# Performance work log

Measured on AMD Instinct MI355X. Metric: run time of the kernel, lower is better.

Reference implementation:

```python
import jax, jax.numpy as jnp
import numpy as np

B, T, C, NH = 4, 2048, 1024, 16
HS = C // NH  # 64


def setup_inputs() -> dict:
    key = jax.random.key(0)
    ks = jax.random.split(key, 3)
    x = jax.random.normal(ks[0], (B, T, C), dtype=jnp.float32)
    w_attn = jax.random.normal(ks[1], (C, 3 * C), dtype=jnp.float32) * (1.0 / np.sqrt(C))
    b_attn = jnp.zeros((3 * C,), dtype=jnp.float32)
    w_proj = jax.random.normal(ks[2], (C, C), dtype=jnp.float32) * (1.0 / np.sqrt(C))
    b_proj = jnp.zeros((C,), dtype=jnp.float32)
    return {"x": x, "w_attn": w_attn, "b_attn": b_attn, "w_proj": w_proj, "b_proj": b_proj}


def reference(x, w_attn, b_attn, w_proj, b_proj):
    Bx, Tx, Cx = x.shape
    qkv = x @ w_attn + b_attn                      # (B,T,3C)
    q, k, v = jnp.split(qkv, 3, axis=2)
    # faithful to torch: view(B,T,hs,nh).transpose(1,3) -> (B,nh,hs,T)
    def to_heads(t):
        return jnp.transpose(t.reshape(Bx, Tx, HS, NH), (0, 3, 2, 1))
    q, k, v = to_heads(q), to_heads(k), to_heads(v)
    # att[b,h,i,j] = q_i . k_j / sqrt(hs)
    att = jnp.einsum('bhdi,bhdj->bhij', q, k) * (1.0 / np.sqrt(HS))
    # buffer is tril.T == upper-triangular; keep i<=j, mask i>j
    keep = jnp.triu(jnp.ones((Tx, Tx), dtype=bool))[None, None]
    att = jnp.where(keep, att, -jnp.inf)
    att = jax.nn.softmax(att, axis=-2)             # normalize over i
    y = jnp.einsum('bhdi,bhij->bhdj', v, att)      # (B,nh,hs,T)
    y = jnp.transpose(y, (0, 3, 2, 1)).reshape(Bx, Tx, Cx)
    return y @ w_proj + b_proj
```

## Files before the change

### kernel.cpp

```cpp
#include <hip/hip_runtime.h>
#include <stdint.h>


typedef __attribute__((ext_vector_type(8))) _Float16 f16x8;
typedef __attribute__((ext_vector_type(4))) _Float16 f16x4;
typedef __attribute__((ext_vector_type(2))) _Float16 h2;
typedef __attribute__((ext_vector_type(2))) __fp16   fp16x2_t;
typedef __attribute__((ext_vector_type(4))) float    f32x4;

#define NT_   8192
#define NC_   1024
#define N3C_  3072

__device__ __forceinline__ uint32_t pkrtz(float a, float b){
  union { fp16x2_t h; uint32_t u; } cv;
  cv.h = __builtin_amdgcn_cvt_pkrtz(a, b);
  return cv.u;
}

__global__ void k_cvt(const float* __restrict__ src, _Float16* __restrict__ dst, int n4){
  int idx = blockIdx.x*blockDim.x + threadIdx.x;
  int stride = gridDim.x*blockDim.x;
  for (int i = idx; i < n4; i += stride){
    float4 v = ((const float4*)src)[i];
    f16x4 o;
    o[0] = (_Float16)v.x; o[1] = (_Float16)v.y;
    o[2] = (_Float16)v.z; o[3] = (_Float16)v.w;
    ((f16x4*)dst)[i] = o;
  }
}

__global__ void k_wattn_t(const float* __restrict__ w, _Float16* __restrict__ wt){
  int t = threadIdx.x;
  int m0 = blockIdx.x*128, c0 = blockIdx.y*32;
  int mcol = m0 + t;
  int part = mcol >> 10, rr = mcol & 1023;
  int mp = part*1024 + (rr & 15)*64 + (rr >> 4);
  alignas(16) _Float16 buf[32];
  #pragma unroll
  for (int cc = 0; cc < 32; cc++)
    buf[cc] = (_Float16)w[(size_t)(c0+cc)*N3C_ + mcol];
  uint4* dst = (uint4*)(wt + (size_t)mp*NC_ + c0);
  const uint4* sb = (const uint4*)buf;
  dst[0]=sb[0]; dst[1]=sb[1]; dst[2]=sb[2]; dst[3]=sb[3];
}

__global__ void k_wproj_t(const float* __restrict__ w, _Float16* __restrict__ wt){
  int t = threadIdx.x;
  int o0 = blockIdx.x*128, cp0 = blockIdx.y*32;
  int o = o0 + t;
  alignas(16) _Float16 buf[32];
  #pragma unroll
  for (int i = 0; i < 32; i++){
    int cp = cp0 + i;
    int row = (cp & 63)*16 + (cp >> 6);
    buf[i] = (_Float16)w[(size_t)row*NC_ + o];
  }
  uint4* dst = (uint4*)(wt + (size_t)o*NC_ + cp0);
  const uint4* sb = (const uint4*)buf;
  dst[0]=sb[0]; dst[1]=sb[1]; dst[2]=sb[2]; dst[3]=sb[3];
}

__global__ void k_bias(const float* __restrict__ ba, float* __restrict__ bp){
  int i = blockIdx.x*blockDim.x + threadIdx.x;
  int part = i >> 10, rr = i & 1023, h = rr >> 6, d = rr & 63;
  bp[i] = ba[part*1024 + d*16 + h];
}

template<int OUT_HALF>
__global__ __launch_bounds__(256) void k_gemm(
    const _Float16* __restrict__ A, const _Float16* __restrict__ BT,
    const float* __restrict__ bias, void* __restrict__ outp,
    _Float16* __restrict__ VTout,
    int M, int N, int K)
{
  __shared__ _Float16 As[128][40];
  __shared__ _Float16 Bs[128][40];
  int tid = threadIdx.x;
  int wave = tid >> 6, lane = tid & 63;
  int wr = wave >> 1, wc = wave & 1;
  int g = lane >> 4, l15 = lane & 15;
  f32x4 acc[4][4] = {};
  const _Float16* Ag = A  + (size_t)blockIdx.y*128*K;
  const _Float16* Bg = BT + (size_t)blockIdx.x*128*K;
  int srow = tid >> 1, skoff = (tid & 1)*16;
  const _Float16* apt = Ag + (size_t)srow*K + skoff;
  const _Float16* bpt = Bg + (size_t)srow*K + skoff;
  uint4 ra0 = *(const uint4*)apt;
  uint4 ra1 = *(const uint4*)(apt + 8);
  uint4 rb0 = *(const uint4*)bpt;
  uint4 rb1 = *(const uint4*)(bpt + 8);
  for (int kt = 0; kt < K; kt += 32){
    __syncthreads();
    *(uint4*)&As[srow][skoff]     = ra0;
    *(uint4*)&As[srow][skoff + 8] = ra1;
    *(uint4*)&Bs[srow][skoff]     = rb0;
    *(uint4*)&Bs[srow][skoff + 8] = rb1;
    __syncthreads();
    if (kt + 32 < K){
      ra0 = *(const uint4*)(apt + kt + 32);
      ra1 = *(const uint4*)(apt + kt + 40);
      rb0 = *(const uint4*)(bpt + kt + 32);
      rb1 = *(const uint4*)(bpt + kt + 40);
    }
    f16x8 af[4], bf[4];
    #pragma unroll
    for (int mi = 0; mi < 4; mi++) af[mi] = *(const f16x8*)&As[wr*64 + mi*16 + l15][g*8];
    #pragma unroll
    for (int ni = 0; ni < 4; ni++) bf[ni] = *(const f16x8*)&Bs[wc*64 + ni*16 + l15][g*8];
    #pragma unroll
    for (int mi = 0; mi < 4; mi++)
      #pragma unroll
      for (int ni = 0; ni < 4; ni++)
        acc[mi][ni] = __builtin_amdgcn_mfma_f32_16x16x32_f16(af[mi], bf[ni], acc[mi][ni], 0, 0, 0);
  }
  int rowBase = blockIdx.y*128 + wr*64;
  int colBase = blockIdx.x*128 + wc*64;
  if (OUT_HALF && colBase >= 2048){
    int b = rowBase >> 11;
    int t0 = (rowBase & 2047);
    #pragma unroll
    for (int mi = 0; mi < 4; mi++){
      #pragma unroll
      for (int ni = 0; ni < 4; ni++){
        int col = colBase + ni*16 + l15;
        int cc = col - 2048;
        int h = cc >> 6, d = cc & 63;
        float bv = bias[col];
        _Float16* dst = VTout + (((size_t)(b*16 + h)*64 + d)*2048) + t0 + mi*16 + g*4;
        f16x4 o;
        #pragma unroll
        for (int r = 0; r < 4; r++) o[r] = (_Float16)(acc[mi][ni][r] + bv);
        *(f16x4*)dst = o;
      }
    }
    return;
  }
  #pragma unroll
  for (int mi = 0; mi < 4; mi++){
    #pragma unroll
    for (int ni = 0; ni < 4; ni++){
      int col = colBase + ni*16 + l15;
      float bv = bias[col];
      #pragma unroll
      for (int r = 0; r < 4; r++){
        int row = rowBase + mi*16 + g*4 + r;
        float v = acc[mi][ni][r] + bv;
        if (OUT_HALF) ((_Float16*)outp)[(size_t)row*N + col] = (_Float16)v;
        else          ((float*)outp)[(size_t)row*N + col] = v;
      }
    }
  }
}

__global__ __launch_bounds__(256) void k_attn(
    const _Float16* __restrict__ qkv, const _Float16* __restrict__ VTb,
    _Float16* __restrict__ Y)
{
  __shared__ _Float16 Ks[2][64][64];
  __shared__ _Float16 Vs[2][64][64];
  __shared__ uint32_t Ps[4][16][32];
  int bid = blockIdx.x;
  int bh = bid & 63;
  int j = bid >> 6;
  const int jts[2] = { j, 31-j };
  int maxjt = 31 - j;
  int b = bh >> 4, h = bh & 15;
  int tid = threadIdx.x, wave = tid >> 6, lane = tid & 63;
  int g = lane >> 4, l15 = lane & 15;
  uint32_t* Pw = &Ps[wave][0][0] + l15*32;
  int xm = (l15 & 7) << 2;
  int swR = (l15 & 7) << 4;
  const _Float16 QS = (_Float16)0.18033688f;
  const float OFF = 12.0f;

  int q0[2];
  f16x8 qf0[2], qf1[2];
  #pragma unroll
  for (int t = 0; t < 2; t++){
    q0[t] = jts[t]*64 + wave*16;
    const _Float16* qp = qkv + (size_t)(b*2048 + q0[t] + l15)*N3C_ + 1024 + h*64;
    qf0[t] = *(const f16x8*)&qp[g*8] * QS;
    qf1[t] = *(const f16x8*)&qp[32 + g*8] * QS;
  }
  float lrun[2] = {0.f, 0.f};
  f32x4 acc[2][4] = {};

  int srow = tid >> 2;
  int sbyte = (tid & 3)*32;
  int swW = (srow & 7) << 4;
  const _Float16* kbase = qkv + (size_t)(b*2048 + srow)*N3C_ + h*64 + (sbyte>>1);
  const _Float16* vbase = VTb + ((size_t)bh*64 + srow)*2048 + (sbyte>>1);

  auto stage = [&](int buf, const uint4& k0, const uint4& k1,
                   const uint4& v0, const uint4& v1){
    char* kw = (char*)&Ks[buf][0][0] + srow*128;
    char* vw = (char*)&Vs[buf][0][0] + srow*128;
    *(uint4*)(kw + ( sbyte       ^ swW)) = k0;
    *(uint4*)(kw + ((sbyte + 16) ^ swW)) = k1;
    *(uint4*)(vw + ( sbyte       ^ swW)) = v0;
    *(uint4*)(vw + ((sbyte + 16) ^ swW)) = v1;
  };

  auto process = [&](const f16x8& qa, const f16x8& qb, float& lr,
                     f32x4* ac, int qt0, int i0, bool diag, int cur){
    const char* kb = (const char*)&Ks[cur][0][0];
    const char* vb = (const char*)&Vs[cur][0][0];
    f32x4 s2[4];
    __builtin_amdgcn_s_setprio(1);
    #pragma unroll
    for (int nb = 0; nb < 4; nb++){
      const char* krow = kb + (nb*16 + l15)*128;
      f16x8 kf0 = *(const f16x8*)(krow + (( g*16)      ^ swR));
      f16x8 kf1 = *(const f16x8*)(krow + ((64 + g*16)  ^ swR));
      f32x4 z = {};
      z = __builtin_amdgcn_mfma_f32_16x16x32_f16(kf0, qa, z, 0, 0, 0);
      z = __builtin_amdgcn_mfma_f32_16x16x32_f16(kf1, qb, z, 0, 0, 0);
      s2[nb] = z;
    }
    __builtin_amdgcn_s_setprio(0);
    float p[16];
    #pragma unroll
    for (int nb = 0; nb < 4; nb++)
      #pragma unroll
      for (int r = 0; r < 4; r++)
        p[nb*4 + r] = s2[nb][r];
    if (diag){
      int qidx = qt0 + l15;
      #pragma unroll
      for (int nb = 0; nb < 4; nb++)
        #pragma unroll
        for (int r = 0; r < 4; r++){
          int kidx = i0 + nb*16 + g*4 + r;
          if (kidx > qidx) p[nb*4 + r] = -3e30f;
        }
    }
    uint32_t pk[8];
    #pragma unroll
    for (int i = 0; i < 8; i++){
      float e0 = __builtin_amdgcn_exp2f(p[2*i]     - OFF);
      float e1 = __builtin_amdgcn_exp2f(p[2*i + 1] - OFF);
      pk[i] = pkrtz(e0, e1);
    }
    #pragma unroll
    for (int nb = 0; nb < 4; nb++)
      #pragma unroll
      for (int r2 = 0; r2 < 2; r2++)
        Pw[(nb*8 + g*2 + r2) ^ xm] = pk[nb*2 + r2];
    __builtin_amdgcn_s_setprio(1);
    #pragma unroll
    for (int ks = 0; ks < 2; ks++){
      f16x8 pb = *(const f16x8*)&Pw[(ks*16 + g*4) ^ xm];
      #pragma unroll
      for (int db = 0; db < 4; db++){
        const char* vrow = vb + (db*16 + l15)*128;
        f16x8 vv = *(const f16x8*)(vrow + ((ks*64 + g*16) ^ swR));
        ac[db] = __builtin_amdgcn_mfma_f32_16x16x32_f16(vv, pb, ac[db], 0, 0, 0);
      }
    }
    __builtin_amdgcn_s_setprio(0);
    const h2 ones = { (_Float16)1.0f, (_Float16)1.0f };
    union { uint32_t u; h2 h; } cv;
    float rs0 = 0.f, rs1 = 0.f;
    #pragma unroll
    for (int i = 0; i < 4; i++){
      cv.u = pk[i];     rs0 = __builtin_amdgcn_fdot2(cv.h, ones, rs0, false);
      cv.u = pk[i + 4]; rs1 = __builtin_amdgcn_fdot2(cv.h, ones, rs1, false);
    }
    lr += rs0 + rs1;
  };

  uint4 ka0 = *(const uint4*)&kbase[0];
  uint4 ka1 = *(const uint4*)&kbase[8];
  uint4 va0 = *(const uint4*)&vbase[0];
  uint4 va1 = *(const uint4*)&vbase[8];
  stage(0, ka0, ka1, va0, va1);
  __syncthreads();
  for (int it = 0; it <= maxjt; ++it){
    int cur = it & 1;
    if (it < maxjt){
      size_t ko = (size_t)(it+1)*64*N3C_;
      int    vo = (it+1)*64;
      ka0 = *(const uint4*)&kbase[ko];
      ka1 = *(const uint4*)&kbase[ko + 8];
      va0 = *(const uint4*)&vbase[vo];
      va1 = *(const uint4*)&vbase[vo + 8];
    }
    process(qf0[1], qf1[1], lrun[1], acc[1], q0[1], it*64, it == jts[1], cur);
    if (it <= jts[0])
      process(qf0[0], qf1[0], lrun[0], acc[0], q0[0], it*64, it == jts[0], cur);
    if (it < maxjt) stage(cur ^ 1, ka0, ka1, va0, va1);
    __syncthreads();
  }

  #pragma unroll
  for (int t = 0; t < 2; t++){
    float rs = lrun[t];
    rs += __shfl_xor(rs, 16);
    rs += __shfl_xor(rs, 32);
    float inv = 1.0f / rs;
    _Float16* yb = Y + (size_t)(b*2048 + q0[t] + l15)*NC_ + h*64 + g*4;
    #pragma unroll
    for (int db = 0; db < 4; db++){
      f16x4 o;
      #pragma unroll
      for (int r = 0; r < 4; r++) o[r] = (_Float16)(acc[t][db][r]*inv);
      *(f16x4*)&yb[db*16] = o;
    }
  }
}

extern "C" void kernel_launch(void* const* d_in, const int* in_sizes, int n_in,
                              void* d_out, int out_size, void* d_ws, size_t ws_size,
                              hipStream_t stream)
{
  const float* x      = (const float*)d_in[0];
  const float* w_attn = (const float*)d_in[1];
  const float* b_attn = (const float*)d_in[2];
  const float* w_proj = (const float*)d_in[3];
  const float* b_proj = (const float*)d_in[4];
  float* out = (float*)d_out;
  char* ws = (char*)d_ws;
  _Float16* xb   = (_Float16*)(ws + 0);
  _Float16* wT   = (_Float16*)(ws + 16777216);
  _Float16* wpT  = (_Float16*)(ws + 23068672);
  float*    bp   = (float*)   (ws + 25165824);
  _Float16* qkv  = (_Float16*)(ws + 25178112);
  _Float16* VT   = (_Float16*)(ws + 75509760);
  _Float16* Y    = (_Float16*)(ws + 92286976);

  k_cvt<<<2048, 256, 0, stream>>>(x, xb, (NT_*NC_)/4);
  k_wattn_t<<<dim3(24, 32), 128, 0, stream>>>(w_attn, wT);
  k_wproj_t<<<dim3(8, 32), 128, 0, stream>>>(w_proj, wpT);
  k_bias<<<12, 256, 0, stream>>>(b_attn, bp);
  k_gemm<1><<<dim3(24, 64), 256, 0, stream>>>(xb, wT, bp, qkv, VT, NT_, N3C_, NC_);
  k_attn<<<1024, 256, 0, stream>>>(qkv, VT, Y);
  k_gemm<0><<<dim3(8, 64), 256, 0, stream>>>(Y, wpT, b_proj, out, (_Float16*)nullptr, NT_, NC_, NC_);
}
```

Before: 191.4 us.

## Use global_load_lds double buffering in GEMM and fuse prep kernels

Replaces register-staged GEMM tile loads with direct global-to-LDS loads into a double-buffered shared tile, so the next K tile streams in while MFMAs run on the current one. Merges the fp32 conversion, weight transposes and bias permutation into a single launch to cut launch overhead. The unpadded LDS layout may add bank conflicts on fragment reads, and every iteration waits on vmcnt(0).

After: 199.5 us. 1.04x slower.

```diff
diff --git a/kernel.cpp b/kernel.cpp
--- a/kernel.cpp
+++ b/kernel.cpp
@@ -17,52 +17,64 @@
   cv.h = __builtin_amdgcn_cvt_pkrtz(a, b);
   return cv.u;
 }
-
-__global__ void k_cvt(const float* __restrict__ src, _Float16* __restrict__ dst, int n4){
-  int idx = blockIdx.x*blockDim.x + threadIdx.x;
-  int stride = gridDim.x*blockDim.x;
-  for (int i = idx; i < n4; i += stride){
-    float4 v = ((const float4*)src)[i];
-    f16x4 o;
-    o[0] = (_Float16)v.x; o[1] = (_Float16)v.y;
-    o[2] = (_Float16)v.z; o[3] = (_Float16)v.w;
-    ((f16x4*)dst)[i] = o;
-  }
-}
-
-__global__ void k_wattn_t(const float* __restrict__ w, _Float16* __restrict__ wt){
-  int t = threadIdx.x;
-  int m0 = blockIdx.x*128, c0 = blockIdx.y*32;
-  int mcol = m0 + t;
-  int part = mcol >> 10, rr = mcol & 1023;
-  int mp = part*1024 + (rr & 15)*64 + (rr >> 4);
-  alignas(16) _Float16 buf[32];
-  #pragma unroll
-  for (int cc = 0; cc < 32; cc++)
-    buf[cc] = (_Float16)w[(size_t)(c0+cc)*N3C_ + mcol];
-  uint4* dst = (uint4*)(wt + (size_t)mp*NC_ + c0);
-  const uint4* sb = (const uint4*)buf;
-  dst[0]=sb[0]; dst[1]=sb[1]; dst[2]=sb[2]; dst[3]=sb[3];
-}
-
-__global__ void k_wproj_t(const float* __restrict__ w, _Float16* __restrict__ wt){
-  int t = threadIdx.x;
-  int o0 = blockIdx.x*128, cp0 = blockIdx.y*32;
-  int o = o0 + t;
-  alignas(16) _Float16 buf[32];
-  #pragma unroll
-  for (int i = 0; i < 32; i++){
-    int cp = cp0 + i;
-    int row = (cp & 63)*16 + (cp >> 6);
-    buf[i] = (_Float16)w[(size_t)row*NC_ + o];
-  }
-  uint4* dst = (uint4*)(wt + (size_t)o*NC_ + cp0);
-  const uint4* sb = (const uint4*)buf;
-  dst[0]=sb[0]; dst[1]=sb[1]; dst[2]=sb[2]; dst[3]=sb[3];
-}
-
-__global__ void k_bias(const float* __restrict__ ba, float* __restrict__ bp){
-  int i = blockIdx.x*blockDim.x + threadIdx.x;
+__device__ __forceinline__ void glds16(const _Float16* g, _Float16* l){
+  __builtin_amdgcn_global_load_lds((const __attribute__((address_space(1))) void*)g,
+                                   (__attribute__((address_space(3))) void*)l, 16, 0, 0);
+}
+
+__global__ __launch_bounds__(256) void k_prep(
+    const float* __restrict__ x, _Float16* __restrict__ xb,
+    const float* __restrict__ wa, _Float16* __restrict__ wT,
+    const float* __restrict__ wp, _Float16* __restrict__ wpT,
+    const float* __restrict__ ba, float* __restrict__ bp)
+{
+  int bid = blockIdx.x, tid = threadIdx.x;
+  if (bid < 2048){
+    int idx = bid*256 + tid, stride = 2048*256;
+    int n4 = (NT_*NC_)/4;
+    for (int i = idx; i < n4; i += stride){
+      float4 v = ((const float4*)x)[i];
+      f16x4 o;
+      o[0] = (_Float16)v.x; o[1] = (_Float16)v.y;
+      o[2] = (_Float16)v.z; o[3] = (_Float16)v.w;
+      ((f16x4*)xb)[i] = o;
+    }
+    return;
+  }
+  if (bid < 2432){
+    int W = (bid - 2048)*2 + (tid >> 7);
+    int t = tid & 127;
+    int m0 = (W / 32)*128, c0 = (W % 32)*32;
+    int mcol = m0 + t;
+    int part = mcol >> 10, rr = mcol & 1023;
+    int mp = part*1024 + (rr & 15)*64 + (rr >> 4);
+    alignas(16) _Float16 buf[32];
+    #pragma unroll
+    for (int cc = 0; cc < 32; cc++)
+      buf[cc] = (_Float16)wa[(size_t)(c0+cc)*N3C_ + mcol];
+    uint4* dst = (uint4*)(wT + (size_t)mp*NC_ + c0);
+    const uint4* sb = (const uint4*)buf;
+    dst[0]=sb[0]; dst[1]=sb[1]; dst[2]=sb[2]; dst[3]=sb[3];
+    return;
+  }
+  if (bid < 2560){
+    int W = (bid - 2432)*2 + (tid >> 7);
+    int t = tid & 127;
+    int o0 = (W / 32)*128, cp0 = (W % 32)*32;
+    int o = o0 + t;
+    alignas(16) _Float16 buf[32];
+    #pragma unroll
+    for (int i = 0; i < 32; i++){
+      int cp = cp0 + i;
+      int row = (cp & 63)*16 + (cp >> 6);
+      buf[i] = (_Float16)wp[(size_t)row*NC_ + o];
+    }
+    uint4* dst = (uint4*)(wpT + (size_t)o*NC_ + cp0);
+    const uint4* sb = (const uint4*)buf;
+    dst[0]=sb[0]; dst[1]=sb[1]; dst[2]=sb[2]; dst[3]=sb[3];
+    return;
+  }
+  int i = (bid - 2560)*256 + tid;
   int part = i >> 10, rr = i & 1023, h = rr >> 6, d = rr & 63;
   bp[i] = ba[part*1024 + d*16 + h];
 }
@@ -74,45 +86,42 @@
     _Float16* __restrict__ VTout,
     int M, int N, int K)
 {
-  __shared__ _Float16 As[128][40];
-  __shared__ _Float16 Bs[128][40];
+  __shared__ _Float16 As[2][128][32];
+  __shared__ _Float16 Bs[2][128][32];
   int tid = threadIdx.x;
   int wave = tid >> 6, lane = tid & 63;
   int wr = wave >> 1, wc = wave & 1;
   int g = lane >> 4, l15 = lane & 15;
   f32x4 acc[4][4] = {};
-  const _Float16* Ag = A  + (size_t)blockIdx.y*128*K;
-  const _Float16* Bg = BT + (size_t)blockIdx.x*128*K;
-  int srow = tid >> 1, skoff = (tid & 1)*16;
-  const _Float16* apt = Ag + (size_t)srow*K + skoff;
-  const _Float16* bpt = Bg + (size_t)srow*K + skoff;
-  uint4 ra0 = *(const uint4*)apt;
-  uint4 ra1 = *(const uint4*)(apt + 8);
-  uint4 rb0 = *(const uint4*)bpt;
-  uint4 rb1 = *(const uint4*)(bpt + 8);
+  int r0 = tid >> 2, cs = (tid & 3)*8;
+  const _Float16* a0 = A  + ((size_t)blockIdx.y*128 + r0)*K + cs;
+  const _Float16* b0 = BT + ((size_t)blockIdx.x*128 + r0)*K + cs;
+  size_t step64 = (size_t)64*K;
+  auto stage = [&](int kt, int buf){
+    glds16(a0 + kt,          &As[buf][r0][cs]);
+    glds16(a0 + kt + step64, &As[buf][r0 + 64][cs]);
+    glds16(b0 + kt,          &Bs[buf][r0][cs]);
+    glds16(b0 + kt + step64, &Bs[buf][r0 + 64][cs]);
+  };
+  stage(0, 0);
+  asm volatile("s_waitcnt vmcnt(0)" ::: "memory");
+  __builtin_amdgcn_s_barrier();
+  int cur = 0;
   for (int kt = 0; kt < K; kt += 32){
-    __syncthreads();
-    *(uint4*)&As[srow][skoff]     = ra0;
-    *(uint4*)&As[srow][skoff + 8] = ra1;
-    *(uint4*)&Bs[srow][skoff]     = rb0;
-    *(uint4*)&Bs[srow][skoff + 8] = rb1;
-    __syncthreads();
-    if (kt + 32 < K){
-      ra0 = *(const uint4*)(apt + kt + 32);
-      ra1 = *(const uint4*)(apt + kt + 40);
-      rb0 = *(const uint4*)(bpt + kt + 32);
-      rb1 = *(const uint4*)(bpt + kt + 40);
-    }
+    if (kt + 32 < K) stage(kt + 32, cur ^ 1);
     f16x8 af[4], bf[4];
     #pragma unroll
-    for (int mi = 0; mi < 4; mi++) af[mi] = *(const f16x8*)&As[wr*64 + mi*16 + l15][g*8];
-    #pragma unroll
-    for (int ni = 0; ni < 4; ni++) bf[ni] = *(const f16x8*)&Bs[wc*64 + ni*16 + l15][g*8];
+    for (int mi = 0; mi < 4; mi++) af[mi] = *(const f16x8*)&As[cur][wr*64 + mi*16 + l15][g*8];
+    #pragma unroll
+    for (int ni = 0; ni < 4; ni++) bf[ni] = *(const f16x8*)&Bs[cur][wc*64 + ni*16 + l15][g*8];
     #pragma unroll
     for (int mi = 0; mi < 4; mi++)
       #pragma unroll
       for (int ni = 0; ni < 4; ni++)
         acc[mi][ni] = __builtin_amdgcn_mfma_f32_16x16x32_f16(af[mi], bf[ni], acc[mi][ni], 0, 0, 0);
+    asm volatile("s_waitcnt vmcnt(0)" ::: "memory");
+    __builtin_amdgcn_s_barrier();
+    cur ^= 1;
   }
   int rowBase = blockIdx.y*128 + wr*64;
   int colBase = blockIdx.x*128 + wc*64;
@@ -329,10 +338,7 @@
   _Float16* VT   = (_Float16*)(ws + 75509760);
   _Float16* Y    = (_Float16*)(ws + 92286976);
 
-  k_cvt<<<2048, 256, 0, stream>>>(x, xb, (NT_*NC_)/4);
-  k_wattn_t<<<dim3(24, 32), 128, 0, stream>>>(w_attn, wT);
-  k_wproj_t<<<dim3(8, 32), 128, 0, stream>>>(w_proj, wpT);
-  k_bias<<<12, 256, 0, stream>>>(b_attn, bp);
+  k_prep<<<2572, 256, 0, stream>>>(x, xb, w_attn, wT, w_proj, wpT, b_attn, bp);
   k_gemm<1><<<dim3(24, 64), 256, 0, stream>>>(xb, wT, bp, qkv, VT, NT_, N3C_, NC_);
   k_attn<<<1024, 256, 0, stream>>>(qkv, VT, Y);
   k_gemm<0><<<dim3(8, 64), 256, 0, stream>>>(Y, wpT, b_proj, out, (_Float16*)nullptr, NT_, NC_, NC_);
```

## Replace QKV GEMM with 256x256-tile kernel using direct global-to-LDS async loads

Applied to the files above, without the earlier changes.

The QKV projection GEMM is replaced with a new kernel that uses 256x256 output tiles on 512 threads. Operands go straight from global memory into a double-buffered, XOR-swizzled LDS layout through global_load_lds, and an explicit vmcnt/barrier schedule overlaps the next tile's loads with MFMA work. MFMA priority is raised around the compute blocks. The aim is more operand reuse per tile and hidden load latency, at the cost of 128KB of LDS per block, a hand-tuned wait schedule that is easy to get wrong, and fewer blocks (384) to fill the CUs.

After: 186.0 us. 1.03x faster.

```diff
diff --git a/kernel.cpp b/kernel.cpp
--- a/kernel.cpp
+++ b/kernel.cpp
@@ -17,6 +17,13 @@
   cv.h = __builtin_amdgcn_cvt_pkrtz(a, b);
   return cv.u;
 }
+__device__ __forceinline__ void glds16(const _Float16* g, _Float16* l){
+  __builtin_amdgcn_global_load_lds((const __attribute__((address_space(1))) void*)g,
+                                   (__attribute__((address_space(3))) void*)l, 16, 0, 0);
+}
+
+#define ASM_VMCNT(N) asm volatile("s_waitcnt vmcnt(" #N ")" ::: "memory")
+#define ASM_BAR()    asm volatile("s_barrier" ::: "memory")
 
 __global__ void k_cvt(const float* __restrict__ src, _Float16* __restrict__ dst, int n4){
   int idx = blockIdx.x*blockDim.x + threadIdx.x;
@@ -67,11 +74,146 @@
   bp[i] = ba[part*1024 + d*16 + h];
 }
 
-template<int OUT_HALF>
-__global__ __launch_bounds__(256) void k_gemm(
+__global__ __launch_bounds__(512, 2) void k_gemm256(
     const _Float16* __restrict__ A, const _Float16* __restrict__ BT,
-    const float* __restrict__ bias, void* __restrict__ outp,
-    _Float16* __restrict__ VTout,
+    const float* __restrict__ bias, _Float16* __restrict__ qkvout,
+    _Float16* __restrict__ VTout)
+{
+  const int K = 1024;
+  __shared__ _Float16 LS[65536];
+  _Float16* As0 = LS;
+  _Float16* As1 = LS + 16384;
+  _Float16* Bs0 = LS + 32768;
+  _Float16* Bs1 = LS + 49152;
+  int tid = threadIdx.x;
+  int w = tid >> 6, lane = tid & 63;
+  int wm = w >> 2, wn = w & 3;
+  int g = lane >> 4, l15 = lane & 15;
+  size_t m0 = (size_t)blockIdx.y * 256;
+  size_t n0 = (size_t)blockIdx.x * 256;
+  f32x4 acc[8][4] = {};
+
+  int srow8 = w*8 + (lane >> 3);
+  int scol  = (((lane & 7) ^ ((lane >> 3) & 7)) << 3);
+  int sdst  = srow8*64 + (lane & 7)*8;
+
+  auto stageA = [&](int tau, int mh){
+    _Float16* dst = (tau & 1) ? As1 : As0;
+    const _Float16* src = A + m0*K + tau*64 + scol;
+    #pragma unroll
+    for (int i = 0; i < 2; i++){
+      int base = i*128 + mh*64;
+      glds16(src + (size_t)(base + srow8)*K, dst + base*64 + sdst);
+    }
+  };
+  auto stageB = [&](int tau, int h){
+    _Float16* dst = (tau & 1) ? Bs1 : Bs0;
+    const _Float16* src = BT + n0*K + tau*64 + scol;
+    #pragma unroll
+    for (int i = 0; i < 2; i++){
+      int base = h*128 + i*64;
+      glds16(src + (size_t)(base + srow8)*K, dst + base*64 + sdst);
+    }
+  };
+
+  const int rcol0 = (g*8) ^ ((l15 & 7) << 3);
+  const int rcol1 = (32 + g*8) ^ ((l15 & 7) << 3);
+  auto readA = [&](int cur, int mh, int kk, f16x8* af){
+    const _Float16* Ap = (cur ? As1 : As0) + (wm*128 + mh*64 + l15)*64
+                         + (kk ? rcol1 : rcol0);
+    #pragma unroll
+    for (int mi = 0; mi < 4; mi++)
+      af[mi] = *(const f16x8*)(Ap + mi*1024);
+  };
+  auto readB = [&](int cur, int kk, f16x8* bf){
+    const _Float16* Bp = (cur ? Bs1 : Bs0) + (wn*64 + l15)*64
+                         + (kk ? rcol1 : rcol0);
+    #pragma unroll
+    for (int ni = 0; ni < 4; ni++)
+      bf[ni] = *(const f16x8*)(Bp + ni*1024);
+  };
+
+#define MFMA16(MH, AF, BF) do {                                               \
+    __builtin_amdgcn_s_setprio(1);                                            \
+    _Pragma("unroll")                                                         \
+    for (int mi = 0; mi < 4; mi++)                                            \
+      _Pragma("unroll")                                                       \
+      for (int ni = 0; ni < 4; ni++)                                          \
+        acc[(MH)*4 + mi][ni] = __builtin_amdgcn_mfma_f32_16x16x32_f16(        \
+            (AF)[mi], (BF)[ni], acc[(MH)*4 + mi][ni], 0, 0, 0);               \
+    __builtin_amdgcn_s_setprio(0);                                            \
+  } while (0)
+
+  stageA(0, 0); stageA(0, 1); stageB(0, 0); stageB(0, 1); stageA(1, 0);
+  ASM_VMCNT(2);
+  ASM_BAR();
+
+  for (int tau = 0; tau < 16; ++tau){
+    int cur = tau & 1;
+    f16x8 af[4], bf[4];
+    readA(cur, 0, 0, af); readB(cur, 0, bf);
+    stageB(tau + 1, 0); stageB(tau + 1, 1);
+    ASM_BAR();
+    MFMA16(0, af, bf);
+    ASM_VMCNT(6); ASM_BAR();
+    readA(cur, 1, 0, af);
+    stageA(tau + 1, 1);
+    ASM_BAR();
+    MFMA16(1, af, bf);
+    ASM_VMCNT(8); ASM_BAR();
+    readA(cur, 0, 1, af); readB(cur, 1, bf);
+    ASM_BAR();
+    MFMA16(0, af, bf);
+    ASM_VMCNT(6); ASM_BAR();
+    readA(cur, 1, 1, af);
+    stageA(tau + 2, 0);
+    ASM_BAR();
+    MFMA16(1, af, bf);
+    ASM_VMCNT(4); ASM_BAR();
+  }
+#undef MFMA16
+
+  int rowBase = (int)m0 + wm*128;
+  int colBase = (int)n0 + wn*64;
+  if (colBase >= 2048){
+    int b = rowBase >> 11;
+    int t0 = rowBase & 2047;
+    #pragma unroll
+    for (int mi = 0; mi < 8; mi++){
+      #pragma unroll
+      for (int ni = 0; ni < 4; ni++){
+        int col = colBase + ni*16 + l15;
+        int cc = col - 2048;
+        int h = cc >> 6, d = cc & 63;
+        float bv = bias[col];
+        _Float16* dst = VTout + (((size_t)(b*16 + h)*64 + d)*2048)
+                        + t0 + mi*16 + g*4;
+        f16x4 o;
+        #pragma unroll
+        for (int r = 0; r < 4; r++) o[r] = (_Float16)(acc[mi][ni][r] + bv);
+        *(f16x4*)dst = o;
+      }
+    }
+    return;
+  }
+  #pragma unroll
+  for (int mi = 0; mi < 8; mi++){
+    #pragma unroll
+    for (int ni = 0; ni < 4; ni++){
+      int col = colBase + ni*16 + l15;
+      float bv = bias[col];
+      #pragma unroll
+      for (int r = 0; r < 4; r++){
+        int row = rowBase + mi*16 + g*4 + r;
+        qkvout[(size_t)row*N3C_ + col] = (_Float16)(acc[mi][ni][r] + bv);
+      }
+    }
+  }
+}
+
+__global__ __launch_bounds__(256) void k_gemm_proj(
+    const _Float16* __restrict__ A, const _Float16* __restrict__ BT,
+    const float* __restrict__ bias, float* __restrict__ outp,
     int M, int N, int K)
 {
   __shared__ _Float16 As[128][40];
@@ -116,26 +258,6 @@
   }
   int rowBase = blockIdx.y*128 + wr*64;
   int colBase = blockIdx.x*128 + wc*64;
-  if (OUT_HALF && colBase >= 2048){
-    int b = rowBase >> 11;
-    int t0 = (rowBase & 2047);
-    #pragma unroll
-    for (int mi = 0; mi < 4; mi++){
-      #pragma unroll
-      for (int ni = 0; ni < 4; ni++){
-        int col = colBase + ni*16 + l15;
-        int cc = col - 2048;
-        int h = cc >> 6, d = cc & 63;
-        float bv = bias[col];
-        _Float16* dst = VTout + (((size_t)(b*16 + h)*64 + d)*2048) + t0 + mi*16 + g*4;
-        f16x4 o;
-        #pragma unroll
-        for (int r = 0; r < 4; r++) o[r] = (_Float16)(acc[mi][ni][r] + bv);
-        *(f16x4*)dst = o;
-      }
-    }
-    return;
-  }
   #pragma unroll
   for (int mi = 0; mi < 4; mi++){
     #pragma unroll
@@ -145,9 +267,7 @@
       #pragma unroll
       for (int r = 0; r < 4; r++){
         int row = rowBase + mi*16 + g*4 + r;
-        float v = acc[mi][ni][r] + bv;
-        if (OUT_HALF) ((_Float16*)outp)[(size_t)row*N + col] = (_Float16)v;
-        else          ((float*)outp)[(size_t)row*N + col] = v;
+        outp[(size_t)row*N + col] = acc[mi][ni][r] + bv;
       }
     }
   }
@@ -333,7 +453,7 @@
   k_wattn_t<<<dim3(24, 32), 128, 0, stream>>>(w_attn, wT);
   k_wproj_t<<<dim3(8, 32), 128, 0, stream>>>(w_proj, wpT);
   k_bias<<<12, 256, 0, stream>>>(b_attn, bp);
-  k_gemm<1><<<dim3(24, 64), 256, 0, stream>>>(xb, wT, bp, qkv, VT, NT_, N3C_, NC_);
+  k_gemm256<<<dim3(12, 32), 512, 0, stream>>>(xb, wT, bp, qkv, VT);
   k_attn<<<1024, 256, 0, stream>>>(qkv, VT, Y);
-  k_gemm<0><<<dim3(8, 64), 256, 0, stream>>>(Y, wpT, b_proj, out, (_Float16*)nullptr, NT_, NC_, NC_);
-}
+  k_gemm_proj<<<dim3(8, 64), 256, 0, stream>>>(Y, wpT, b_proj, out, NT_, NC_, NC_);
+}
```

## Widen GEMM tile to 128x256 and feed P from registers in attention

Applied to the files above, without the earlier changes.

The GEMM kernel now uses 512 threads with a 128x256 output tile, which doubles B-tile reuse per A load and halves the grid. Attention's P·V step uses the 16x16x16 f16 MFMA, so the packed softmax probabilities go straight from registers as the B operand. This drops the per-wave LDS staging of P and its synchronisation. The cost is more MFMA instructions with smaller K, larger GEMM blocks that may reduce occupancy, and a grid of fewer blocks.

Result: slower. 201.2 us (+5.1%).

```diff
diff --git a/kernel.cpp b/kernel.cpp
--- a/kernel.cpp
+++ b/kernel.cpp
@@ -11,6 +11,16 @@
 #define NT_   8192
 #define NC_   1024
 #define N3C_  3072
+
+#if __has_builtin(__builtin_amdgcn_mfma_f32_16x16x16f16)
+#define MFMA_K16(a,b,c) __builtin_amdgcn_mfma_f32_16x16x16f16((a),(b),(c),0,0,0)
+#define HAVE_K16 1
+#elif __has_builtin(__builtin_amdgcn_mfma_f32_16x16x16_f16)
+#define MFMA_K16(a,b,c) __builtin_amdgcn_mfma_f32_16x16x16_f16((a),(b),(c),0,0,0)
+#define HAVE_K16 1
+#else
+#define HAVE_K16 0
+#endif
 
 __device__ __forceinline__ uint32_t pkrtz(float a, float b){
   union { fp16x2_t h; uint32_t u; } cv;
@@ -68,54 +78,52 @@
 }
 
 template<int OUT_HALF>
-__global__ __launch_bounds__(256) void k_gemm(
+__global__ __launch_bounds__(512) void k_gemm(
     const _Float16* __restrict__ A, const _Float16* __restrict__ BT,
     const float* __restrict__ bias, void* __restrict__ outp,
     _Float16* __restrict__ VTout,
     int M, int N, int K)
 {
   __shared__ _Float16 As[128][40];
-  __shared__ _Float16 Bs[128][40];
+  __shared__ _Float16 Bs[256][40];
   int tid = threadIdx.x;
-  int wave = tid >> 6, lane = tid & 63;
-  int wr = wave >> 1, wc = wave & 1;
+  int w = tid >> 6, lane = tid & 63;
+  int wm = w >> 2, wn = w & 3;
   int g = lane >> 4, l15 = lane & 15;
   f32x4 acc[4][4] = {};
   const _Float16* Ag = A  + (size_t)blockIdx.y*128*K;
-  const _Float16* Bg = BT + (size_t)blockIdx.x*128*K;
-  int srow = tid >> 1, skoff = (tid & 1)*16;
-  const _Float16* apt = Ag + (size_t)srow*K + skoff;
-  const _Float16* bpt = Bg + (size_t)srow*K + skoff;
-  uint4 ra0 = *(const uint4*)apt;
-  uint4 ra1 = *(const uint4*)(apt + 8);
+  const _Float16* Bg = BT + (size_t)blockIdx.x*256*K;
+  int srA = tid >> 2, skA = (tid & 3)*8;
+  int srB = tid >> 1, skB = (tid & 1)*16;
+  const _Float16* apt = Ag + (size_t)srA*K + skA;
+  const _Float16* bpt = Bg + (size_t)srB*K + skB;
+  uint4 ra  = *(const uint4*)apt;
   uint4 rb0 = *(const uint4*)bpt;
   uint4 rb1 = *(const uint4*)(bpt + 8);
   for (int kt = 0; kt < K; kt += 32){
     __syncthreads();
-    *(uint4*)&As[srow][skoff]     = ra0;
-    *(uint4*)&As[srow][skoff + 8] = ra1;
-    *(uint4*)&Bs[srow][skoff]     = rb0;
-    *(uint4*)&Bs[srow][skoff + 8] = rb1;
+    *(uint4*)&As[srA][skA]      = ra;
+    *(uint4*)&Bs[srB][skB]      = rb0;
+    *(uint4*)&Bs[srB][skB + 8]  = rb1;
     __syncthreads();
     if (kt + 32 < K){
-      ra0 = *(const uint4*)(apt + kt + 32);
-      ra1 = *(const uint4*)(apt + kt + 40);
+      ra  = *(const uint4*)(apt + kt + 32);
       rb0 = *(const uint4*)(bpt + kt + 32);
       rb1 = *(const uint4*)(bpt + kt + 40);
     }
     f16x8 af[4], bf[4];
     #pragma unroll
-    for (int mi = 0; mi < 4; mi++) af[mi] = *(const f16x8*)&As[wr*64 + mi*16 + l15][g*8];
-    #pragma unroll
-    for (int ni = 0; ni < 4; ni++) bf[ni] = *(const f16x8*)&Bs[wc*64 + ni*16 + l15][g*8];
+    for (int mi = 0; mi < 4; mi++) af[mi] = *(const f16x8*)&As[wm*64 + mi*16 + l15][g*8];
+    #pragma unroll
+    for (int ni = 0; ni < 4; ni++) bf[ni] = *(const f16x8*)&Bs[wn*64 + ni*16 + l15][g*8];
     #pragma unroll
     for (int mi = 0; mi < 4; mi++)
       #pragma unroll
       for (int ni = 0; ni < 4; ni++)
         acc[mi][ni] = __builtin_amdgcn_mfma_f32_16x16x32_f16(af[mi], bf[ni], acc[mi][ni], 0, 0, 0);
   }
-  int rowBase = blockIdx.y*128 + wr*64;
-  int colBase = blockIdx.x*128 + wc*64;
+  int rowBase = blockIdx.y*128 + wm*64;
+  int colBase = blockIdx.x*256 + wn*64;
   if (OUT_HALF && colBase >= 2048){
     int b = rowBase >> 11;
     int t0 = (rowBase & 2047);
@@ -159,7 +167,9 @@
 {
   __shared__ _Float16 Ks[2][64][64];
   __shared__ _Float16 Vs[2][64][64];
+#if !HAVE_K16
   __shared__ uint32_t Ps[4][16][32];
+#endif
   int bid = blockIdx.x;
   int bh = bid & 63;
   int j = bid >> 6;
@@ -168,8 +178,10 @@
   int b = bh >> 4, h = bh & 15;
   int tid = threadIdx.x, wave = tid >> 6, lane = tid & 63;
   int g = lane >> 4, l15 = lane & 15;
+#if !HAVE_K16
   uint32_t* Pw = &Ps[wave][0][0] + l15*32;
   int xm = (l15 & 7) << 2;
+#endif
   int swR = (l15 & 7) << 4;
   const _Float16 QS = (_Float16)0.18033688f;
   const float OFF = 12.0f;
@@ -242,6 +254,21 @@
       float e1 = __builtin_amdgcn_exp2f(p[2*i + 1] - OFF);
       pk[i] = pkrtz(e0, e1);
     }
+#if HAVE_K16
+    __builtin_amdgcn_s_setprio(1);
+    #pragma unroll
+    for (int nb = 0; nb < 4; nb++){
+      union { uint32_t u[2]; f16x4 hv; } pb;
+      pb.u[0] = pk[nb*2]; pb.u[1] = pk[nb*2 + 1];
+      #pragma unroll
+      for (int db = 0; db < 4; db++){
+        const char* vrow = vb + (db*16 + l15)*128;
+        f16x4 vv = *(const f16x4*)(vrow + ((nb*32 + g*8) ^ swR));
+        ac[db] = MFMA_K16(vv, pb.hv, ac[db]);
+      }
+    }
+    __builtin_amdgcn_s_setprio(0);
+#else
     #pragma unroll
     for (int nb = 0; nb < 4; nb++)
       #pragma unroll
@@ -259,6 +286,7 @@
       }
     }
     __builtin_amdgcn_s_setprio(0);
+#endif
     const h2 ones = { (_Float16)1.0f, (_Float16)1.0f };
     union { uint32_t u; h2 h; } cv;
     float rs0 = 0.f, rs1 = 0.f;
@@ -333,7 +361,7 @@
   k_wattn_t<<<dim3(24, 32), 128, 0, stream>>>(w_attn, wT);
   k_wproj_t<<<dim3(8, 32), 128, 0, stream>>>(w_proj, wpT);
   k_bias<<<12, 256, 0, stream>>>(b_attn, bp);
-  k_gemm<1><<<dim3(24, 64), 256, 0, stream>>>(xb, wT, bp, qkv, VT, NT_, N3C_, NC_);
+  k_gemm<1><<<dim3(12, 64), 512, 0, stream>>>(xb, wT, bp, qkv, VT, NT_, N3C_, NC_);
   k_attn<<<1024, 256, 0, stream>>>(qkv, VT, Y);
-  k_gemm<0><<<dim3(8, 64), 256, 0, stream>>>(Y, wpT, b_proj, out, (_Float16*)nullptr, NT_, NC_, NC_);
-}
+  k_gemm<0><<<dim3(4, 64), 512, 0, stream>>>(Y, wpT, b_proj, out, (_Float16*)nullptr, NT_, NC_, NC_);
+}
```
